# Optimization experiments

Hardware: AMD Instinct MI355X
Metric: run time of the kernel (lower is better)

The kernel has to match this reference:

```python
import jax, jax.numpy as jnp
import numpy as np

N_TASKS = 32
D = 2097152  # flattened gradient dim
MAX_ITER = 250
STOP_CRIT = 1e-6
EPS = 1e-8


def setup_inputs() -> dict:
    key = jax.random.key(0)
    vecs = jax.random.normal(key, (N_TASKS, D), dtype=jnp.float32)
    return {"vecs": vecs}


def _line_solver(v11, v12, v22):
    # min-norm point on the segment between two vectors (vectorized / scalar)
    g = (v22 - v12) / (v11 + v22 - 2.0 * v12 + EPS)
    c = v22 + g * (v12 - v22)
    gamma = jnp.where(v12 >= v22, 0.0, g)
    gamma = jnp.where(v12 >= v11, 1.0, gamma)
    cost = jnp.where(v12 >= v22, v22, c)
    cost = jnp.where(v12 >= v11, v11, cost)
    return gamma, cost


def _planar_init(G, n):
    iu_np, ju_np = np.triu_indices(n, 1)
    iu = jnp.asarray(iu_np)
    ju = jnp.asarray(ju_np)
    vivj = G[iu, ju]
    vivi = G[iu, iu]
    vjvj = G[ju, ju]
    gamma, cost = _line_solver(vivi, vivj, vjvj)
    off = jnp.argmin(cost)
    sol = jnp.zeros(n, dtype=G.dtype)
    sol = sol.at[iu[off]].set(gamma[off]).at[ju[off]].set(1.0 - gamma[off])
    return sol


def _proj_simplex(gamma, i_grid):
    s = jnp.sort(gamma)[::-1]  # descending
    tmp_max = (jnp.cumsum(s) - 1.0) / i_grid
    cond = tmp_max[:-1] > s[1:]
    first = jnp.argmax(cond)  # index of first True (0 if none)
    tmax = jnp.where(jnp.any(cond), tmp_max[:-1][first], tmp_max[-1])
    return jnp.maximum(gamma - tmax, 0.0)


def _next_point(cur, grad, n, i_grid):
    proj = grad - jnp.sum(grad) / n
    neg = proj < 0
    pos = proj > 0
    tm1 = jnp.where(neg, -cur / jnp.where(neg, proj, 1.0), jnp.inf)
    tm2 = jnp.where(pos, (1.0 - cur) / jnp.where(pos, proj, 1.0), jnp.inf)
    m1 = jnp.min(jnp.where(tm1 > 1e-7, tm1, jnp.inf))
    t = jnp.where(jnp.isfinite(m1), m1, 1.0)
    m2 = jnp.min(jnp.where(tm2 > 1e-7, tm2, jnp.inf))
    t = jnp.minimum(t, m2)  # no-op if m2 is inf
    nxt = proj * t + cur
    return _proj_simplex(nxt, i_grid)


def reference(vecs):
    n = vecs.shape[0]
    G = vecs @ vecs.T  # [n, n] grammian; only memory-heavy step
    sol0 = _planar_init(G, n)
    i_grid = jnp.arange(n, dtype=G.dtype) + 1.0
    n_f = jnp.asarray(n, dtype=G.dtype)

    def body(carry, _):
        sol, done = carry
        grad_dir = -(G @ sol)
        newp = _next_point(sol, grad_dir, n_f, i_grid)
        Gs = G @ sol
        Gn = G @ newp
        v11 = sol @ Gs
        v12 = sol @ Gn
        v22 = newp @ Gn
        gamma, _ = _line_solver(v11, v12, v22)
        new_sol = gamma * sol + (1.0 - gamma) * newp
        stop = jnp.sum(jnp.abs(new_sol - sol)) < STOP_CRIT
        nd = done | stop
        # original returns the OLD sol_vec when change < stop_crit
        out = jnp.where(nd, sol, new_sol)
        return (out, nd), None

    (sol, _), _ = jax.lax.scan(body, (sol0, jnp.array(False)), None, length=MAX_ITER)
    return sol
```

## Files before the change

### kernel.cpp

```cpp
#include <hip/hip_runtime.h>

#define NT 32
#define EPSF 1e-8f

#define TILE_COLS 64
#define GR_THREADS 256
#define WAVES_PB 4
#define TILES_PW 8

__global__ __launch_bounds__(GR_THREADS, 2)
void gram_kernel(const float* __restrict__ vecs, double* __restrict__ Gd, int D)
{
    __shared__ __align__(16) float tile[WAVES_PB][TILE_COLS * 32];
    __shared__ float Gpart[NT * NT];

    const int tid  = threadIdx.x;
    const int wave = tid >> 6;
    const int lane = tid & 63;

    for (int e = tid; e < NT * NT; e += GR_THREADS) Gpart[e] = 0.0f;
    __syncthreads();

    float* my = tile[wave];
    const int swz = lane & 7;

    const int cj = lane >> 4;
    const int pi = (lane >> 2) & 3;
    const int pk = lane & 3;

    float acc[8][8];
#pragma unroll
    for (int r = 0; r < 8; r++)
#pragma unroll
        for (int c = 0; c < 8; c++) acc[r][c] = 0.0f;

    const unsigned base0 = (unsigned)blockIdx.x * (WAVES_PB * TILES_PW * TILE_COLS)
                         + (unsigned)wave * (TILES_PW * TILE_COLS) + (unsigned)lane;

    for (int t = 0; t < TILES_PW; t++) {
        const unsigned off = base0 + (unsigned)t * TILE_COLS;
#pragma unroll
        for (int g = 0; g < 8; g++) {
            const float* r0 = vecs + (size_t)(4 * g + 0) * (size_t)D;
            const float* r1 = vecs + (size_t)(4 * g + 1) * (size_t)D;
            const float* r2 = vecs + (size_t)(4 * g + 2) * (size_t)D;
            const float* r3 = vecs + (size_t)(4 * g + 3) * (size_t)D;
            float4 w = make_float4(r0[off], r1[off], r2[off], r3[off]);
            *(float4*)(my + lane * 32 + ((g ^ swz) << 2)) = w;
        }
#pragma unroll
        for (int jt = 0; jt < 16; jt++) {
            const int j = (jt << 2) + cj;
            const float* col = my + j * 32;
            const int js = j & 7;
            const float4 a0 = *(const float4*)(col + (((2 * pi) ^ js) << 2));
            const float4 a1 = *(const float4*)(col + (((2 * pi + 1) ^ js) << 2));
            const float4 b0 = *(const float4*)(col + (((2 * pk) ^ js) << 2));
            const float4 b1 = *(const float4*)(col + (((2 * pk + 1) ^ js) << 2));
            const float a[8] = {a0.x, a0.y, a0.z, a0.w, a1.x, a1.y, a1.z, a1.w};
            const float b[8] = {b0.x, b0.y, b0.z, b0.w, b1.x, b1.y, b1.z, b1.w};
#pragma unroll
            for (int r = 0; r < 8; r++)
#pragma unroll
                for (int c = 0; c < 8; c++)
                    acc[r][c] = fmaf(a[r], b[c], acc[r][c]);
        }
    }

#pragma unroll
    for (int r = 0; r < 8; r++)
#pragma unroll
        for (int c = 0; c < 8; c++) {
            float v = acc[r][c];
            v += __shfl_xor(v, 16);
            v += __shfl_xor(v, 32);
            if (lane < 16)
                atomicAdd(&Gpart[(8 * pi + r) * NT + (8 * pk + c)], v);
        }
    __syncthreads();
    for (int e = tid; e < NT * NT; e += GR_THREADS)
        atomicAdd(&Gd[e], (double)Gpart[e]);
}

template<int CTRL>
__device__ __forceinline__ float dpp0(float x) {
    return __int_as_float(__builtin_amdgcn_update_dpp(
        0, __float_as_int(x), CTRL, 0xF, 0xF, true));
}
template<int CTRL>
__device__ __forceinline__ float dppk(float oldv, float x) {
    return __int_as_float(__builtin_amdgcn_update_dpp(
        __float_as_int(oldv), __float_as_int(x), CTRL, 0xF, 0xF, false));
}
__device__ __forceinline__ float rdlane(float x, int l) {
    return __int_as_float(__builtin_amdgcn_readlane(__float_as_int(x), l));
}
__device__ __forceinline__ unsigned long long rdlane64(unsigned long long x, int l) {
    int lo = __builtin_amdgcn_readlane((int)(unsigned int)x, l);
    int hi = __builtin_amdgcn_readlane((int)(unsigned int)(x >> 32), l);
    return ((unsigned long long)(unsigned int)hi << 32) | (unsigned int)lo;
}
template<int CTRL>
__device__ __forceinline__ unsigned long long dpp64k(unsigned long long x) {
    int lo = (int)(unsigned int)x, hi = (int)(unsigned int)(x >> 32);
    int plo = __builtin_amdgcn_update_dpp(lo, lo, CTRL, 0xF, 0xF, false);
    int phi = __builtin_amdgcn_update_dpp(hi, hi, CTRL, 0xF, 0xF, false);
    return ((unsigned long long)(unsigned int)phi << 32) | (unsigned int)plo;
}

__device__ __forceinline__ float bsum32u(float v) {
    v += dpp0<0x111>(v);
    v += dpp0<0x112>(v);
    v += dpp0<0x114>(v);
    v += dpp0<0x118>(v);
    return rdlane(v, 15) + rdlane(v, 31);
}
__device__ __forceinline__ float bmin32u(float v) {
    v = fminf(v, dppk<0x111>(v, v));
    v = fminf(v, dppk<0x112>(v, v));
    v = fminf(v, dppk<0x114>(v, v));
    v = fminf(v, dppk<0x118>(v, v));
    return fminf(rdlane(v, 15), rdlane(v, 31));
}
__device__ __forceinline__ unsigned long long bminu64(unsigned long long P) {
    { unsigned long long q = dpp64k<0x111>(P); P = (q < P) ? q : P; }
    { unsigned long long q = dpp64k<0x112>(P); P = (q < P) ? q : P; }
    { unsigned long long q = dpp64k<0x114>(P); P = (q < P) ? q : P; }
    { unsigned long long q = dpp64k<0x118>(P); P = (q < P) ? q : P; }
    unsigned long long a = rdlane64(P, 0);
    unsigned long long b = rdlane64(P, 16);
    return (a < b) ? a : b;
}

__global__ __launch_bounds__(64)
void solver_kernel(const double* __restrict__ Gd, float* __restrict__ out)
{
    __shared__ float Gsh[NT * 33];
    const int lane = threadIdx.x;

    for (int t2 = 0; t2 < 16; t2++) {
        int e = t2 * 64 + lane;
        Gsh[(e >> 5) * 33 + (e & 31)] = (float)Gd[e];
    }
    __syncthreads();

    float Grow[NT];
#pragma unroll
    for (int k = 0; k < NT; k++)
        Grow[k] = (lane < NT) ? Gsh[lane * 33 + k] : 0.0f;

    float bestCost = INFINITY, bestGamma = 0.0f;
    int bestEnc = 0x7FFFFFFF;
    for (int a = 0; a < NT - 1; a++) {
        int b = a + 1 + lane;
        if (b < NT) {
            float v11 = Gsh[a * 33 + a];
            float v12 = Gsh[a * 33 + b];
            float v22 = Gsh[b * 33 + b];
            float g = (v22 - v12) / (v11 + v22 - 2.0f * v12 + EPSF);
            float c = v22 + g * (v12 - v22);
            float gamma = (v12 >= v22) ? 0.0f : g;
            float cost  = (v12 >= v22) ? v22 : c;
            if (v12 >= v11) { gamma = 1.0f; cost = v11; }
            int enc = a * NT + b;
            if (cost < bestCost) { bestCost = cost; bestEnc = enc; bestGamma = gamma; }
        }
    }
#pragma unroll
    for (int m = 1; m < 64; m <<= 1) {
        float oc = __shfl_xor(bestCost, m);
        int   oe = __shfl_xor(bestEnc, m);
        float og = __shfl_xor(bestGamma, m);
        if (oc < bestCost || (oc == bestCost && oe < bestEnc)) {
            bestCost = oc; bestEnc = oe; bestGamma = og;
        }
    }
    const int bi = bestEnc >> 5, bj = bestEnc & 31;

    float sol = 0.0f;
    if (lane == bi) sol = bestGamma;
    if (lane == bj) sol = 1.0f - bestGamma;

    float Gsol;
    {
        float s0 = 0, s1 = 0, s2 = 0, s3 = 0;
#pragma unroll
        for (int k = 0; k < NT; k += 4) {
            s0 = fmaf(Grow[k + 0], rdlane(sol, k + 0), s0);
            s1 = fmaf(Grow[k + 1], rdlane(sol, k + 1), s1);
            s2 = fmaf(Grow[k + 2], rdlane(sol, k + 2), s2);
            s3 = fmaf(Grow[k + 3], rdlane(sol, k + 3), s3);
        }
        Gsol = (s0 + s1) + (s2 + s3);
    }

    for (int it = 0; it < 250; it++) {
        float grad = -Gsol;
        float proj = grad - bsum32u(grad) * 0.03125f;

        float tm1 = (proj < 0.0f) ? (-sol / proj) : INFINITY;
        float tm2 = (proj > 0.0f) ? ((1.0f - sol) / proj) : INFINITY;
        float m1 = bmin32u((tm1 > 1e-7f) ? tm1 : INFINITY);
        float m2 = bmin32u((tm2 > 1e-7f) ? tm2 : INFINITY);
        float t = __builtin_isinf(m1) ? 1.0f : m1;
        t = fminf(t, m2);
        float nxt = fmaf(proj, t, sol);

        int nb = __float_as_int(nxt);
        unsigned int u = (unsigned int)nb ^ ((nb < 0) ? 0xFFFFFFFFu : 0x80000000u);
        unsigned long long Ki = ((unsigned long long)u << 6)
                              | (unsigned long long)(63 - lane);

        int rank = 0;
        float S = 0.0f;
#pragma unroll
        for (int j = 0; j < 32; j++) {
            unsigned int uj = (unsigned int)__builtin_amdgcn_readlane((int)u, j);
            float vj = rdlane(nxt, j);
            unsigned long long Kj = ((unsigned long long)uj << 6)
                                  | (unsigned long long)(63 - j);
            bool gt = Kj > Ki;
            rank += gt ? 1 : 0;
            S += gt ? vj : 0.0f;
        }
        float total = bsum32u(nxt);

        float cand = (S - 1.0f) / (float)rank;
        bool cond = (rank >= 1) && (cand > nxt);
        unsigned long long P =
            ((unsigned long long)(cond ? (unsigned)rank : 0xFFu) << 32)
            | (unsigned int)__float_as_int(cand);
        unsigned long long M = bminu64(P);
        float tmax = ((unsigned int)(M >> 32) == 0xFFu)
                   ? (total - 1.0f) * 0.03125f
                   : __int_as_float((int)(unsigned int)M);
        float newp = fmaxf(nxt - tmax, 0.0f);
        if (lane >= NT) newp = 0.0f;

        float n0 = 0, n1 = 0, n2 = 0, n3 = 0;
#pragma unroll
        for (int k = 0; k < NT; k += 4) {
            n0 = fmaf(Grow[k + 0], rdlane(newp, k + 0), n0);
            n1 = fmaf(Grow[k + 1], rdlane(newp, k + 1), n1);
            n2 = fmaf(Grow[k + 2], rdlane(newp, k + 2), n2);
            n3 = fmaf(Grow[k + 3], rdlane(newp, k + 3), n3);
        }
        float Gn = (n0 + n1) + (n2 + n3);

        float v11 = bsum32u(sol * Gsol);
        float v12 = bsum32u(sol * Gn);
        float v22 = bsum32u(newp * Gn);

        float g = (v22 - v12) / (v11 + v22 - 2.0f * v12 + EPSF);
        float gamma = (v12 >= v22) ? 0.0f : g;
        gamma = (v12 >= v11) ? 1.0f : gamma;

        float new_sol = gamma * sol + (1.0f - gamma) * newp;
        float diff = bsum32u(fabsf(new_sol - sol));
        if (diff < 1e-6f) break;
        sol = new_sol;
        Gsol = fmaf(gamma, Gsol - Gn, Gn);
    }
    if (lane < NT) out[lane] = sol;
}

extern "C" void kernel_launch(void* const* d_in, const int* in_sizes, int n_in,
                              void* d_out, int out_size, void* d_ws, size_t ws_size,
                              hipStream_t stream) {
    const float* vecs = (const float*)d_in[0];
    float* out = (float*)d_out;
    double* Gd = (double*)d_ws;
    const int D = in_sizes[0] / NT;

    hipMemsetAsync(Gd, 0, NT * NT * sizeof(double), stream);

    const int cols_per_block = WAVES_PB * TILES_PW * TILE_COLS;
    const int grid = D / cols_per_block;
    gram_kernel<<<grid, GR_THREADS, 0, stream>>>(vecs, Gd, D);
    solver_kernel<<<1, 64, 0, stream>>>(Gd, out);
}
```

Baseline: 433.3 us.

## Prefetch next gram tile into registers and split solver work across both half-waves

The gram kernel now loads the next tile's 32 row values into registers while the current tile is being computed, and its launch bound drops to one block per SM so the extra registers fit. The solver kernel duplicates the 32-element state across both 32-lane halves. It does the matvec and the sort-rank counting half-by-half through LDS instead of 32 readlane calls, and recomputes G·sol each iteration rather than updating it incrementally. It also merges the v11 and v22 reductions into one DPP pass. The aim is to hide global load latency and shorten the serial solver iteration, at the cost of higher register pressure and lower occupancy in the gram kernel.

```diff
diff --git a/kernel.cpp b/kernel.cpp
--- a/kernel.cpp
+++ b/kernel.cpp
@@ -8,7 +8,7 @@
 #define WAVES_PB 4
 #define TILES_PW 8
 
-__global__ __launch_bounds__(GR_THREADS, 2)
+__global__ __launch_bounds__(GR_THREADS, 1)
 void gram_kernel(const float* __restrict__ vecs, double* __restrict__ Gd, int D)
 {
     __shared__ __align__(16) float tile[WAVES_PB][TILE_COLS * 32];
@@ -37,16 +37,23 @@
     const unsigned base0 = (unsigned)blockIdx.x * (WAVES_PB * TILES_PW * TILE_COLS)
                          + (unsigned)wave * (TILES_PW * TILE_COLS) + (unsigned)lane;
 
+    float pre[32];
+#pragma unroll
+    for (int r = 0; r < 32; r++)
+        pre[r] = (vecs + (size_t)r * (size_t)D)[base0];
+
     for (int t = 0; t < TILES_PW; t++) {
-        const unsigned off = base0 + (unsigned)t * TILE_COLS;
 #pragma unroll
         for (int g = 0; g < 8; g++) {
-            const float* r0 = vecs + (size_t)(4 * g + 0) * (size_t)D;
-            const float* r1 = vecs + (size_t)(4 * g + 1) * (size_t)D;
-            const float* r2 = vecs + (size_t)(4 * g + 2) * (size_t)D;
-            const float* r3 = vecs + (size_t)(4 * g + 3) * (size_t)D;
-            float4 w = make_float4(r0[off], r1[off], r2[off], r3[off]);
+            float4 w = make_float4(pre[4 * g + 0], pre[4 * g + 1],
+                                   pre[4 * g + 2], pre[4 * g + 3]);
             *(float4*)(my + lane * 32 + ((g ^ swz) << 2)) = w;
+        }
+        if (t + 1 < TILES_PW) {
+            const unsigned off = base0 + (unsigned)(t + 1) * TILE_COLS;
+#pragma unroll
+            for (int r = 0; r < 32; r++)
+                pre[r] = (vecs + (size_t)r * (size_t)D)[off];
         }
 #pragma unroll
         for (int jt = 0; jt < 16; jt++) {
@@ -127,8 +134,8 @@
     { unsigned long long q = dpp64k<0x112>(P); P = (q < P) ? q : P; }
     { unsigned long long q = dpp64k<0x114>(P); P = (q < P) ? q : P; }
     { unsigned long long q = dpp64k<0x118>(P); P = (q < P) ? q : P; }
-    unsigned long long a = rdlane64(P, 0);
-    unsigned long long b = rdlane64(P, 16);
+    unsigned long long a = rdlane64(P, 15);
+    unsigned long long b = rdlane64(P, 31);
     return (a < b) ? a : b;
 }
 
@@ -136,18 +143,35 @@
 void solver_kernel(const double* __restrict__ Gd, float* __restrict__ out)
 {
     __shared__ float Gsh[NT * 33];
+    __shared__ float  Tvec[64];
+    __shared__ float2 Tkv[64];
+
     const int lane = threadIdx.x;
+    const int e = lane & 31;
+    const int h = lane >> 5;
 
     for (int t2 = 0; t2 < 16; t2++) {
-        int e = t2 * 64 + lane;
-        Gsh[(e >> 5) * 33 + (e & 31)] = (float)Gd[e];
+        int idx = t2 * 64 + lane;
+        Gsh[(idx >> 5) * 33 + (idx & 31)] = (float)Gd[idx];
     }
     __syncthreads();
 
-    float Grow[NT];
-#pragma unroll
-    for (int k = 0; k < NT; k++)
-        Grow[k] = (lane < NT) ? Gsh[lane * 33 + k] : 0.0f;
+    float Grow[16];
+#pragma unroll
+    for (int k = 0; k < 16; k++)
+        Grow[k] = Gsh[e * 33 + 16 * h + k];
+
+    auto matvec = [&](float x) -> float {
+        Tvec[lane] = x;
+        float a0 = 0.0f, a1 = 0.0f;
+#pragma unroll
+        for (int s = 0; s < 16; s += 2) {
+            a0 = fmaf(Grow[s + 0], Tvec[16 * h + s + 0], a0);
+            a1 = fmaf(Grow[s + 1], Tvec[16 * h + s + 1], a1);
+        }
+        float half = a0 + a1;
+        return half + __shfl_xor(half, 32);
+    };
 
     float bestCost = INFINITY, bestGamma = 0.0f;
     int bestEnc = 0x7FFFFFFF;
@@ -178,23 +202,12 @@
     const int bi = bestEnc >> 5, bj = bestEnc & 31;
 
     float sol = 0.0f;
-    if (lane == bi) sol = bestGamma;
-    if (lane == bj) sol = 1.0f - bestGamma;
-
-    float Gsol;
-    {
-        float s0 = 0, s1 = 0, s2 = 0, s3 = 0;
-#pragma unroll
-        for (int k = 0; k < NT; k += 4) {
-            s0 = fmaf(Grow[k + 0], rdlane(sol, k + 0), s0);
-            s1 = fmaf(Grow[k + 1], rdlane(sol, k + 1), s1);
-            s2 = fmaf(Grow[k + 2], rdlane(sol, k + 2), s2);
-            s3 = fmaf(Grow[k + 3], rdlane(sol, k + 3), s3);
-        }
-        Gsol = (s0 + s1) + (s2 + s3);
-    }
+    if (e == bi) sol = bestGamma;
+    if (e == bj) sol = 1.0f - bestGamma;
 
     for (int it = 0; it < 250; it++) {
+        float Gsol = matvec(sol);
+
         float grad = -Gsol;
         float proj = grad - bsum32u(grad) * 0.03125f;
 
@@ -207,22 +220,23 @@
         float nxt = fmaf(proj, t, sol);
 
         int nb = __float_as_int(nxt);
-        unsigned int u = (unsigned int)nb ^ ((nb < 0) ? 0xFFFFFFFFu : 0x80000000u);
-        unsigned long long Ki = ((unsigned long long)u << 6)
-                              | (unsigned long long)(63 - lane);
+        unsigned u = (unsigned)nb ^ ((nb < 0) ? 0xFFFFFFFFu : 0x80000000u);
+        Tkv[lane] = make_float2(nxt, __int_as_float((int)u));
 
         int rank = 0;
         float S = 0.0f;
-#pragma unroll
-        for (int j = 0; j < 32; j++) {
-            unsigned int uj = (unsigned int)__builtin_amdgcn_readlane((int)u, j);
-            float vj = rdlane(nxt, j);
-            unsigned long long Kj = ((unsigned long long)uj << 6)
-                                  | (unsigned long long)(63 - j);
-            bool gt = Kj > Ki;
+        const int dtie = e - 16 * h;
+#pragma unroll
+        for (int s = 0; s < 16; s++) {
+            float2 kv = Tkv[16 * h + s];
+            unsigned uj = (unsigned)__float_as_int(kv.y);
+            bool gt = (uj > u) || ((uj == u) && (s < dtie));
             rank += gt ? 1 : 0;
-            S += gt ? vj : 0.0f;
-        }
+            S += gt ? kv.x : 0.0f;
+        }
+        rank += __shfl_xor(rank, 32);
+        S += __shfl_xor(S, 32);
+
         float total = bsum32u(nxt);
 
         float cand = (S - 1.0f) / (float)rank;
@@ -235,21 +249,17 @@
                    ? (total - 1.0f) * 0.03125f
                    : __int_as_float((int)(unsigned int)M);
         float newp = fmaxf(nxt - tmax, 0.0f);
-        if (lane >= NT) newp = 0.0f;
-
-        float n0 = 0, n1 = 0, n2 = 0, n3 = 0;
-#pragma unroll
-        for (int k = 0; k < NT; k += 4) {
-            n0 = fmaf(Grow[k + 0], rdlane(newp, k + 0), n0);
-            n1 = fmaf(Grow[k + 1], rdlane(newp, k + 1), n1);
-            n2 = fmaf(Grow[k + 2], rdlane(newp, k + 2), n2);
-            n3 = fmaf(Grow[k + 3], rdlane(newp, k + 3), n3);
-        }
-        float Gn = (n0 + n1) + (n2 + n3);
-
-        float v11 = bsum32u(sol * Gsol);
+
+        float Gn = matvec(newp);
+
+        float z = (h == 0) ? (sol * Gsol) : (newp * Gn);
+        z += dpp0<0x111>(z);
+        z += dpp0<0x112>(z);
+        z += dpp0<0x114>(z);
+        z += dpp0<0x118>(z);
+        float v11 = rdlane(z, 15) + rdlane(z, 31);
+        float v22 = rdlane(z, 47) + rdlane(z, 63);
         float v12 = bsum32u(sol * Gn);
-        float v22 = bsum32u(newp * Gn);
 
         float g = (v22 - v12) / (v11 + v22 - 2.0f * v12 + EPSF);
         float gamma = (v12 >= v22) ? 0.0f : g;
@@ -259,7 +269,6 @@
         float diff = bsum32u(fabsf(new_sol - sol));
         if (diff < 1e-6f) break;
         sol = new_sol;
-        Gsol = fmaf(gamma, Gsol - Gn, Gn);
     }
     if (lane < NT) out[lane] = sol;
 }
```

Result: faster. 408.9 us (-5.6%).
